# Kernel optimization log

Measured on AMD Instinct MI355X. Metric: run time of the kernel, lower is better.

## Reference

```python
import jax, jax.numpy as jnp
import numpy as np

MAXU = 6          # init arg maxU
MAXV = 6          # init arg maxV (ratio=None)
TRUNC = 4         # cfg.TRUNCATED_SIZE; cfg.TRUNCATED=True, cfg.FLOW_REG_BY_MAX=True


def setup_inputs() -> dict:
    key = jax.random.key(0)
    B, H, W = 8, 128, 160
    U, V = 2 * MAXU + 1, 2 * MAXV + 1
    x = jax.random.normal(key, (B, 1, U, V, H, W), dtype=jnp.float32)
    return {"x": x}


def reference(x):
    # x: [B,1,U,V,H,W] cost volume
    x = x[:, 0]                                   # [B,U,V,H,W]
    b, u, v, h, w = x.shape

    # --- truncation mask (cfg.TRUNCATED) ---
    # argmax over flattened (u,v); scatter one-hot + MaxPool3d((2t+1,2t+1,1))
    # is equivalent to a +-t box around the per-pixel argmax location.
    idx = jnp.argmax(x.reshape(b, u * v, h, w), axis=1)   # [B,H,W] int
    ui = (idx // v)[:, None, None]                        # [B,1,1,H,W]
    vi = (idx % v)[:, None, None]
    ugrid = jnp.arange(u).reshape(1, u, 1, 1, 1)
    vgrid = jnp.arange(v).reshape(1, 1, v, 1, 1)
    mask = (jnp.abs(ugrid - ui) <= TRUNC) & (jnp.abs(vgrid - vi) <= TRUNC)
    xm = jnp.where(mask, x, -jnp.inf)

    # --- softmax over the U*V displacement hypotheses (FLOW_REG_BY_MAX) ---
    p = jax.nn.softmax(xm.reshape(b, u * v, h, w), axis=1).reshape(b, u, v, h, w)

    dispU = jnp.arange(-MAXU, MAXU + 1, dtype=x.dtype)    # [U]
    dispV = jnp.arange(-MAXV, MAXV + 1, dtype=x.dtype)    # [V]
    flowU = jnp.einsum('buvhw,u->bhw', p, dispU)
    flowV = jnp.einsum('buvhw,v->bhw', p, dispV)
    return jnp.stack((flowU, flowV), axis=1)              # [B,2,H,W]
```

## Files before the change

### kernel.cpp

```cpp
#include <hip/hip_runtime.h>
#include <math.h>

#define Vdim 13
#define HW 20480
#define UV 169
#define TRUNC 4
#define NPIX (8 * HW)
#define PPB 64
#define NPL 43

__global__ __launch_bounds__(256, 4) void flow_regression_kernel(
    const float* __restrict__ x, float* __restrict__ out) {
    int t    = threadIdx.x;
    int wave = t >> 6;
    int lane = t & 63;
    int q    = lane >> 4;
    int pcol = (wave << 4) | (lane & 15);
    int pix0 = blockIdx.x * PPB;
    int b    = pix0 / HW;
    int hw   = pix0 - b * HW + pcol;
    int base_pl = q * NPL;

    const float* gp = x + (size_t)b * UV * HW + hw;

    float vals[NPL];
    #pragma unroll
    for (int i = 0; i < 40; ++i)
        vals[i] = gp[(size_t)(base_pl + i) * HW];
    #pragma unroll
    for (int i = 40; i < NPL; ++i) {
        int pl   = base_pl + i;
        bool pad = pl >= UV;
        float v  = gp[(size_t)(pad ? (UV - 1) : pl) * HW];
        vals[i]  = pad ? -INFINITY : v;
    }
    #pragma unroll
    for (int i = 0; i < NPL; ++i) asm volatile("" : "+v"(vals[i]));

    float m = vals[0];
    int  mi = base_pl;
    #pragma unroll
    for (int i = 1; i < NPL; ++i)
        if (vals[i] > m) { m = vals[i]; mi = base_pl + i; }
    {
        float om = __shfl_xor(m, 16); int oi = __shfl_xor(mi, 16);
        if (om > m || (om == m && oi < mi)) { m = om; mi = oi; }
        om = __shfl_xor(m, 32); oi = __shfl_xor(mi, 32);
        if (om > m || (om == m && oi < mi)) { m = om; mi = oi; }
    }
    int ui = (mi * 158) >> 11;
    int vi = mi - ui * Vdim;

    float s = 0.f, su = 0.f, sv = 0.f;
    int u = 3 * q, v = 4 * q;
    #pragma unroll
    for (int i = 0; i < NPL; ++i) {
        bool in = (u - ui <= TRUNC) && (ui - u <= TRUNC) &&
                  (v - vi <= TRUNC) && (vi - v <= TRUNC);
        float e = in ? __expf(vals[i] - m) : 0.f;
        s  += e;
        su += e * (float)(u - 6);
        sv += e * (float)(v - 6);
        if (++v == Vdim) { v = 0; ++u; }
    }
    s  += __shfl_xor(s, 16);  su += __shfl_xor(su, 16);  sv += __shfl_xor(sv, 16);
    s  += __shfl_xor(s, 32);  su += __shfl_xor(su, 32);  sv += __shfl_xor(sv, 32);

    if (q == 0) {
        float inv = 1.0f / s;
        float* ob = out + (size_t)b * 2 * HW + hw;
        ob[0]  = su * inv;
        ob[HW] = sv * inv;
    }
}

extern "C" void kernel_launch(void* const* d_in, const int* in_sizes, int n_in,
                              void* d_out, int out_size, void* d_ws, size_t ws_size,
                              hipStream_t stream) {
    const float* x = (const float*)d_in[0];
    float* out = (float*)d_out;
    flow_regression_kernel<<<NPIX / PPB, 256, 0, stream>>>(x, out);
}
```

Measured before the change: 165.7 us.

## Process four pixels per thread with float4 loads and stores

Result: slower. 228.6 us (+38.0%).

```diff
diff --git a/kernel.cpp b/kernel.cpp
--- a/kernel.cpp
+++ b/kernel.cpp
@@ -4,73 +4,99 @@
 #define Vdim 13
 #define HW 20480
 #define UV 169
-#define TRUNC 4
 #define NPIX (8 * HW)
-#define PPB 64
 #define NPL 43
 
-__global__ __launch_bounds__(256, 4) void flow_regression_kernel(
+__global__ __launch_bounds__(256, 2) void flow_regression_kernel(
     const float* __restrict__ x, float* __restrict__ out) {
     int t    = threadIdx.x;
     int wave = t >> 6;
     int lane = t & 63;
     int q    = lane >> 4;
-    int pcol = (wave << 4) | (lane & 15);
-    int pix0 = blockIdx.x * PPB;
+    int pix0 = blockIdx.x * 256 + wave * 64 + (lane & 15) * 4;
     int b    = pix0 / HW;
-    int hw   = pix0 - b * HW + pcol;
+    int hw   = pix0 - b * HW;
     int base_pl = q * NPL;
 
     const float* gp = x + (size_t)b * UV * HW + hw;
 
-    float vals[NPL];
+    float va[4][NPL];
     #pragma unroll
-    for (int i = 0; i < 40; ++i)
-        vals[i] = gp[(size_t)(base_pl + i) * HW];
+    for (int i = 0; i < 40; ++i) {
+        const float4 v4 = *(const float4*)(gp + (size_t)(base_pl + i) * HW);
+        va[0][i] = v4.x; va[1][i] = v4.y; va[2][i] = v4.z; va[3][i] = v4.w;
+    }
     #pragma unroll
     for (int i = 40; i < NPL; ++i) {
         int pl   = base_pl + i;
         bool pad = pl >= UV;
-        float v  = gp[(size_t)(pad ? (UV - 1) : pl) * HW];
-        vals[i]  = pad ? -INFINITY : v;
+        const float4 v4 = *(const float4*)(gp + (size_t)(pad ? (UV - 1) : pl) * HW);
+        va[0][i] = pad ? -INFINITY : v4.x;
+        va[1][i] = pad ? -INFINITY : v4.y;
+        va[2][i] = pad ? -INFINITY : v4.z;
+        va[3][i] = pad ? -INFINITY : v4.w;
     }
     #pragma unroll
-    for (int i = 0; i < NPL; ++i) asm volatile("" : "+v"(vals[i]));
+    for (int i = 0; i < NPL; ++i)
+        asm volatile("" : "+v"(va[0][i]), "+v"(va[1][i]),
+                          "+v"(va[2][i]), "+v"(va[3][i]));
 
-    float m = vals[0];
-    int  mi = base_pl;
+    float m[4]; int mi[4];
+    #pragma unroll
+    for (int j = 0; j < 4; ++j) { m[j] = va[j][0]; mi[j] = base_pl; }
     #pragma unroll
     for (int i = 1; i < NPL; ++i)
-        if (vals[i] > m) { m = vals[i]; mi = base_pl + i; }
-    {
-        float om = __shfl_xor(m, 16); int oi = __shfl_xor(mi, 16);
-        if (om > m || (om == m && oi < mi)) { m = om; mi = oi; }
-        om = __shfl_xor(m, 32); oi = __shfl_xor(mi, 32);
-        if (om > m || (om == m && oi < mi)) { m = om; mi = oi; }
+        #pragma unroll
+        for (int j = 0; j < 4; ++j)
+            if (va[j][i] > m[j]) { m[j] = va[j][i]; mi[j] = base_pl + i; }
+    #pragma unroll
+    for (int j = 0; j < 4; ++j) {
+        float om = __shfl_xor(m[j], 16); int oi = __shfl_xor(mi[j], 16);
+        if (om > m[j] || (om == m[j] && oi < mi[j])) { m[j] = om; mi[j] = oi; }
+        om = __shfl_xor(m[j], 32); oi = __shfl_xor(mi[j], 32);
+        if (om > m[j] || (om == m[j] && oi < mi[j])) { m[j] = om; mi[j] = oi; }
     }
-    int ui = (mi * 158) >> 11;
-    int vi = mi - ui * Vdim;
+    int ui[4], vi[4];
+    #pragma unroll
+    for (int j = 0; j < 4; ++j) {
+        ui[j] = (mi[j] * 158) >> 11;
+        vi[j] = mi[j] - ui[j] * Vdim;
+    }
 
-    float s = 0.f, su = 0.f, sv = 0.f;
+    float s[4]  = {0.f, 0.f, 0.f, 0.f};
+    float su[4] = {0.f, 0.f, 0.f, 0.f};
+    float sv[4] = {0.f, 0.f, 0.f, 0.f};
     int u = 3 * q, v = 4 * q;
     #pragma unroll
     for (int i = 0; i < NPL; ++i) {
-        bool in = (u - ui <= TRUNC) && (ui - u <= TRUNC) &&
-                  (v - vi <= TRUNC) && (vi - v <= TRUNC);
-        float e = in ? __expf(vals[i] - m) : 0.f;
-        s  += e;
-        su += e * (float)(u - 6);
-        sv += e * (float)(v - 6);
+        float du = (float)(u - 6), dv = (float)(v - 6);
+        #pragma unroll
+        for (int j = 0; j < 4; ++j) {
+            bool in = ((unsigned)(u - ui[j] + 4) <= 8u) &&
+                      ((unsigned)(v - vi[j] + 4) <= 8u);
+            float e = in ? __expf(va[j][i] - m[j]) : 0.f;
+            s[j]  += e;
+            su[j] += e * du;
+            sv[j] += e * dv;
+        }
         if (++v == Vdim) { v = 0; ++u; }
     }
-    s  += __shfl_xor(s, 16);  su += __shfl_xor(su, 16);  sv += __shfl_xor(sv, 16);
-    s  += __shfl_xor(s, 32);  su += __shfl_xor(su, 32);  sv += __shfl_xor(sv, 32);
+    #pragma unroll
+    for (int j = 0; j < 4; ++j) {
+        s[j]  += __shfl_xor(s[j], 16);  s[j]  += __shfl_xor(s[j], 32);
+        su[j] += __shfl_xor(su[j], 16); su[j] += __shfl_xor(su[j], 32);
+        sv[j] += __shfl_xor(sv[j], 16); sv[j] += __shfl_xor(sv[j], 32);
+    }
 
     if (q == 0) {
-        float inv = 1.0f / s;
+        float4 oU, oV;
+        oU.x = su[0] / s[0]; oU.y = su[1] / s[1];
+        oU.z = su[2] / s[2]; oU.w = su[3] / s[3];
+        oV.x = sv[0] / s[0]; oV.y = sv[1] / s[1];
+        oV.z = sv[2] / s[2]; oV.w = sv[3] / s[3];
         float* ob = out + (size_t)b * 2 * HW + hw;
-        ob[0]  = su * inv;
-        ob[HW] = sv * inv;
+        *(float4*)ob        = oU;
+        *(float4*)(ob + HW) = oV;
     }
 }
 
@@ -79,5 +105,5 @@
                               hipStream_t stream) {
     const float* x = (const float*)d_in[0];
     float* out = (float*)d_out;
-    flow_regression_kernel<<<NPIX / PPB, 256, 0, stream>>>(x, out);
+    flow_regression_kernel<<<NPIX / 256, 256, 0, stream>>>(x, out);
 }
```
